# Performance work log

Hardware: AMD Instinct MI355X
Metric: run time of the kernel (lower is better)

## Reference

```python
import jax, jax.numpy as jnp
import numpy as np

INPUT_DIM = 20000
UNITS = 4096
NNZ = 800000
BATCH = 1024


def setup_inputs() -> dict:
    key = jax.random.key(0)
    k1, k2, k3, k4 = jax.random.split(key, 4)
    x = jax.random.normal(k1, (BATCH, INPUT_DIM), dtype=jnp.float32)
    kernel_vector = jax.random.normal(k2, (NNZ,), dtype=jnp.float32) * 0.05
    bias = jnp.zeros((UNITS,), dtype=jnp.float32)
    rows = jax.random.randint(k3, (NNZ,), 0, INPUT_DIM, dtype=jnp.int32)
    cols = jax.random.randint(k4, (NNZ,), 0, UNITS, dtype=jnp.int32)
    nonzero_ind = jnp.stack([rows, cols], axis=1)  # [NNZ, 2]
    return {"x": x, "kernel_vector": kernel_vector, "bias": bias, "nonzero_ind": nonzero_ind}


def reference(x, kernel_vector, bias, nonzero_ind):
    # scatter_nd: build dense (input_dim, units) kernel; duplicates accumulate (matches tf.scatter_nd)
    input_dim = x.shape[1]
    units = bias.shape[0]
    dense_kernel = jnp.zeros((input_dim, units), dtype=kernel_vector.dtype)
    dense_kernel = dense_kernel.at[nonzero_ind[:, 0], nonzero_ind[:, 1]].add(kernel_vector)
    out = jnp.matmul(x, dense_kernel) + bias  # [B, units]
    return jnp.tanh(out)
```

## Files before the change

### kernel.cpp

```cpp
#include <hip/hip_runtime.h>
#include <hip/hip_fp16.h>

#define BATCH      1024
#define INPUT_DIM  20000
#define UNITS      4096
#define NNZ        800000
#define BAND_ROW   10000
#define CAP        192
#define NSLOT      (UNITS * 2)

#define WS_XT     0
#define WS_CNT    40960000
#define WS_PAIRS  (WS_CNT + 32768)
#define ZERO_INTS (NSLOT + NSLOT * CAP * 2)

__global__ __launch_bounds__(256) void transpose_in_kernel(
    const float4* __restrict__ x4, unsigned int* __restrict__ xTu,
    uint2* __restrict__ zbase) {
    int t = threadIdx.x;
    unsigned int gid = (blockIdx.y * gridDim.x + blockIdx.x) * 256 + t;
    if (gid < ZERO_INTS / 2) zbase[gid] = make_uint2(0u, 0u);

    __shared__ float tile[64][33];
    int d0 = blockIdx.x * 32;
    int b0 = blockIdx.y * 64;

    int fx = t & 7, rr = t >> 3;
#pragma unroll
    for (int p = 0; p < 2; p++) {
        int b = rr + p * 32;
        float4 v = x4[(size_t)(b0 + b) * (INPUT_DIM / 4) + (d0 >> 2) + fx];
        tile[b][fx * 4 + 0] = v.x; tile[b][fx * 4 + 1] = v.y;
        tile[b][fx * 4 + 2] = v.z; tile[b][fx * 4 + 3] = v.w;
    }
    __syncthreads();
    int bq = t & 15, dd = t >> 4;
#pragma unroll
    for (int p = 0; p < 2; p++) {
        int d = dd + p * 16;
        unsigned short h0 = __half_as_ushort(__float2half(tile[bq * 4 + 0][d]));
        unsigned short h1 = __half_as_ushort(__float2half(tile[bq * 4 + 1][d]));
        unsigned short h2 = __half_as_ushort(__float2half(tile[bq * 4 + 2][d]));
        unsigned short h3 = __half_as_ushort(__float2half(tile[bq * 4 + 3][d]));
        uint2 u = make_uint2((unsigned)h0 | ((unsigned)h1 << 16),
                             (unsigned)h2 | ((unsigned)h3 << 16));
        *(uint2*)(xTu + (size_t)(d0 + d) * (BATCH / 2) + (b0 >> 1) + bq * 2) = u;
    }
}

__global__ void scatter_kernel(const int2* __restrict__ ind2, const float* __restrict__ vals_in,
                               int* __restrict__ cnt, uint2* __restrict__ pairs) {
    int i = blockIdx.x * blockDim.x + threadIdx.x;
    if (i < NNZ) {
        int2 rc = ind2[i];
        int band = (rc.x >= BAND_ROW) ? 1 : 0;
        int slot = (rc.y << 1) + band;
        int pos = atomicAdd(&cnt[slot], 1);
        if (pos < CAP)
            pairs[slot * CAP + pos] =
                make_uint2((unsigned)rc.x << 11, __float_as_uint(vals_in[i]));
    }
}

__device__ __forceinline__ void accum8(uint4 q, float v, float* a) {
    const __half2* h = (const __half2*)&q;
#pragma unroll
    for (int i = 0; i < 4; i++) {
        a[2 * i]     = fmaf(__half2float(__low2half(h[i])),  v, a[2 * i]);
        a[2 * i + 1] = fmaf(__half2float(__high2half(h[i])), v, a[2 * i + 1]);
    }
}

__global__ __launch_bounds__(512, 8) void spmm_kernel(
    const uint2* __restrict__ pairs, const int* __restrict__ cnt,
    const char* __restrict__ xTb, const float* __restrict__ bias,
    float* __restrict__ out) {
    __shared__ float tile[128][17];
    int bid = blockIdx.x;
    int kLow = bid & 7;
    int cg = bid >> 3;
    int tid = threadIdx.x;
    int lane = tid & 63;
    int w = tid >> 6;
    int g = lane >> 4;
    int s = lane & 15;
    unsigned int laneterm = (unsigned)(kLow << 8) + (unsigned)(s << 4);
    int colbase = (cg << 4) + (w << 1);

    float a[2][8] = {{0.f,0.f,0.f,0.f,0.f,0.f,0.f,0.f},
                     {0.f,0.f,0.f,0.f,0.f,0.f,0.f,0.f}};
#pragma unroll
    for (int bd = 0; bd < 2; ++bd) {
#pragma unroll
        for (int c = 0; c < 2; ++c) {
            int slot = ((colbase + c) << 1) + bd;
            int n = cnt[slot];
            if (n > CAP) n = CAP;
            int npad = (n + 7) & ~7;
            const uint2* pb = pairs + slot * CAP + g;
            float* ac = a[c];
            for (int j = 0; j < npad; j += 8) {
                uint2 e0 = pb[j];
                uint2 e1 = pb[j + 4];
                uint4 q0 = *(const uint4*)(xTb + (e0.x + laneterm));
                uint4 q1 = *(const uint4*)(xTb + (e1.x + laneterm));
                accum8(q0, __uint_as_float(e0.y), ac);
                accum8(q1, __uint_as_float(e1.y), ac);
            }
        }
    }

#pragma unroll
    for (int c = 0; c < 2; ++c) {
        float bc = bias[colbase + c];
#pragma unroll
        for (int i = 0; i < 8; i++) {
            float v = a[c][i];
            v += __shfl_xor(v, 16, 64);
            v += __shfl_xor(v, 32, 64);
            if (g == 0)
                tile[(s << 3) + i][(w << 1) + c] = tanhf(v + bc);
        }
    }
    __syncthreads();

    int bl = tid >> 2;
    int c0 = (tid & 3) << 2;
    float4 vv = make_float4(tile[bl][c0], tile[bl][c0 + 1],
                            tile[bl][c0 + 2], tile[bl][c0 + 3]);
    *(float4*)(out + (size_t)((kLow << 7) + bl) * UNITS + (cg << 4) + c0) = vv;
}

extern "C" void kernel_launch(void* const* d_in, const int* in_sizes, int n_in,
                              void* d_out, int out_size, void* d_ws, size_t ws_size,
                              hipStream_t stream) {
    const float* x    = (const float*)d_in[0];
    const float* vals = (const float*)d_in[1];
    const float* bias = (const float*)d_in[2];
    const int*   ind  = (const int*)d_in[3];
    float* out = (float*)d_out;

    char* ws = (char*)d_ws;
    char*  xT    = ws + WS_XT;
    int*   cnt   = (int*)(ws + WS_CNT);
    uint2* pairs = (uint2*)(ws + WS_PAIRS);

    transpose_in_kernel<<<dim3(INPUT_DIM / 32, BATCH / 64), 256, 0, stream>>>(
        (const float4*)x, (unsigned int*)xT, (uint2*)(ws + WS_CNT));
    scatter_kernel<<<NNZ / 256, 256, 0, stream>>>((const int2*)ind, vals, cnt, pairs);
    spmm_kernel<<<2048, 512, 0, stream>>>(pairs, cnt, xT, bias, out);
}
```

Measured before the change: 294.2 us.

## Fuse scatter with transpose, split zeroing, prefetch pair entries in SpMM loop

Zeroing of the count/pairs buffers moves into its own small kernel. The scatter and the x transpose/fp16 conversion now run as one launch, with separate block ranges doing each job. This lets the atomic scatter overlap the bandwidth-bound transpose and removes one launch. In the SpMM kernel, the four slot counts are read with a single vector load, and the next pair entries are software-prefetched so their index loads overlap the gather. This adds one more launch for zeroing, which must finish before the scatter, and more register pressure in the SpMM loop.

```diff
diff --git a/kernel.cpp b/kernel.cpp
--- a/kernel.cpp
+++ b/kernel.cpp
@@ -13,17 +13,38 @@
 #define WS_CNT    40960000
 #define WS_PAIRS  (WS_CNT + 32768)
 #define ZERO_INTS (NSLOT + NSLOT * CAP * 2)
+#define ZERO_U4   (ZERO_INTS / 4)
+#define SCAT_BLK  (NNZ / 256)
+#define TR_BLK    ((INPUT_DIM / 32) * (BATCH / 64))
 
-__global__ __launch_bounds__(256) void transpose_in_kernel(
-    const float4* __restrict__ x4, unsigned int* __restrict__ xTu,
-    uint2* __restrict__ zbase) {
+__global__ __launch_bounds__(256) void zero_kernel(uint4* __restrict__ z) {
+    unsigned int gid = blockIdx.x * 256 + threadIdx.x;
+    z[gid] = make_uint4(0u, 0u, 0u, 0u);
+}
+
+__global__ __launch_bounds__(256) void fused_prep_kernel(
+    const int2* __restrict__ ind2, const float* __restrict__ vals_in,
+    int* __restrict__ cnt, uint2* __restrict__ pairs,
+    const float4* __restrict__ x4, unsigned int* __restrict__ xTu) {
+    __shared__ float tile[64][33];
     int t = threadIdx.x;
-    unsigned int gid = (blockIdx.y * gridDim.x + blockIdx.x) * 256 + t;
-    if (gid < ZERO_INTS / 2) zbase[gid] = make_uint2(0u, 0u);
+    int bid = blockIdx.x;
 
-    __shared__ float tile[64][33];
-    int d0 = blockIdx.x * 32;
-    int b0 = blockIdx.y * 64;
+    if (bid < SCAT_BLK) {
+        int i = bid * 256 + t;
+        int2 rc = ind2[i];
+        int band = (rc.x >= BAND_ROW) ? 1 : 0;
+        int slot = (rc.y << 1) + band;
+        int pos = atomicAdd(&cnt[slot], 1);
+        if (pos < CAP)
+            pairs[slot * CAP + pos] =
+                make_uint2((unsigned)rc.x << 11, __float_as_uint(vals_in[i]));
+        return;
+    }
+
+    int tb = bid - SCAT_BLK;
+    int d0 = (tb % 625) * 32;
+    int b0 = (tb / 625) * 64;
 
     int fx = t & 7, rr = t >> 3;
 #pragma unroll
@@ -45,20 +66,6 @@
         uint2 u = make_uint2((unsigned)h0 | ((unsigned)h1 << 16),
                              (unsigned)h2 | ((unsigned)h3 << 16));
         *(uint2*)(xTu + (size_t)(d0 + d) * (BATCH / 2) + (b0 >> 1) + bq * 2) = u;
-    }
-}
-
-__global__ void scatter_kernel(const int2* __restrict__ ind2, const float* __restrict__ vals_in,
-                               int* __restrict__ cnt, uint2* __restrict__ pairs) {
-    int i = blockIdx.x * blockDim.x + threadIdx.x;
-    if (i < NNZ) {
-        int2 rc = ind2[i];
-        int band = (rc.x >= BAND_ROW) ? 1 : 0;
-        int slot = (rc.y << 1) + band;
-        int pos = atomicAdd(&cnt[slot], 1);
-        if (pos < CAP)
-            pairs[slot * CAP + pos] =
-                make_uint2((unsigned)rc.x << 11, __float_as_uint(vals_in[i]));
     }
 }
 
@@ -87,25 +94,36 @@
     unsigned int laneterm = (unsigned)(kLow << 8) + (unsigned)(s << 4);
     int colbase = (cg << 4) + (w << 1);
 
+    int base2 = colbase << 1;
+    int4 c4 = *(const int4*)(cnt + base2);
+    int ncnt[4] = {c4.x, c4.y, c4.z, c4.w};
+
     float a[2][8] = {{0.f,0.f,0.f,0.f,0.f,0.f,0.f,0.f},
                      {0.f,0.f,0.f,0.f,0.f,0.f,0.f,0.f}};
 #pragma unroll
     for (int bd = 0; bd < 2; ++bd) {
 #pragma unroll
         for (int c = 0; c < 2; ++c) {
-            int slot = ((colbase + c) << 1) + bd;
-            int n = cnt[slot];
+            int slot = base2 + 2 * c + bd;
+            int n = ncnt[2 * c + bd];
             if (n > CAP) n = CAP;
             int npad = (n + 7) & ~7;
             const uint2* pb = pairs + slot * CAP + g;
             float* ac = a[c];
+            if (npad == 0) continue;
+            uint2 e0 = pb[0];
+            uint2 e1 = pb[4];
             for (int j = 0; j < npad; j += 8) {
-                uint2 e0 = pb[j];
-                uint2 e1 = pb[j + 4];
                 uint4 q0 = *(const uint4*)(xTb + (e0.x + laneterm));
                 uint4 q1 = *(const uint4*)(xTb + (e1.x + laneterm));
-                accum8(q0, __uint_as_float(e0.y), ac);
-                accum8(q1, __uint_as_float(e1.y), ac);
+                float v0 = __uint_as_float(e0.y);
+                float v1 = __uint_as_float(e1.y);
+                if (j + 8 < npad) {
+                    e0 = pb[j + 8];
+                    e1 = pb[j + 12];
+                }
+                accum8(q0, v0, ac);
+                accum8(q1, v1, ac);
             }
         }
     }
@@ -145,8 +163,8 @@
     int*   cnt   = (int*)(ws + WS_CNT);
     uint2* pairs = (uint2*)(ws + WS_PAIRS);
 
-    transpose_in_kernel<<<dim3(INPUT_DIM / 32, BATCH / 64), 256, 0, stream>>>(
-        (const float4*)x, (unsigned int*)xT, (uint2*)(ws + WS_CNT));
-    scatter_kernel<<<NNZ / 256, 256, 0, stream>>>((const int2*)ind, vals, cnt, pairs);
+    zero_kernel<<<ZERO_U4 / 256, 256, 0, stream>>>((uint4*)(ws + WS_CNT));
+    fused_prep_kernel<<<SCAT_BLK + TR_BLK, 256, 0, stream>>>(
+        (const int2*)ind, vals, cnt, pairs, (const float4*)x, (unsigned int*)xT);
     spmm_kernel<<<2048, 512, 0, stream>>>(pairs, cnt, xT, bias, out);
 }
```

Measured after the change: 285.6 us. 2.9% less time.
